# Optimization experiments

Hardware: AMD Instinct MI355X
Metric: run time of the kernel (lower is better)

Reference implementation:

```python
import jax, jax.numpy as jnp
import numpy as np

B, P, R, H, M, A = 2048, 2048, 4096, 6, 256, 256
TAU, BETA = 0.1, 5.0


def setup_inputs() -> dict:
    key = jax.random.key(0)
    ks = jax.random.split(key, 12)
    M_minus = jax.random.uniform(ks[0], (B, M), dtype=jnp.float32)
    # rank-0 actions as sparse binary mask over predicates
    action_mask = (jax.random.uniform(ks[1], (B, P)) < 0.01).astype(jnp.float32)
    # temporal gate per (microstep, rule): 0/1
    gate = (jax.random.uniform(ks[2], (B, R)) < 0.7).astype(jnp.float32)
    body_idx = jax.random.randint(ks[3], (R, H), 0, P, dtype=jnp.int32)
    body_mask = (jax.random.uniform(ks[4], (R, H)) < 0.6).astype(jnp.float32)
    body_mask = body_mask.at[:, 0].set(1.0)  # every rule has >=1 body atom
    head_idx = jax.random.randint(ks[5], (R,), 0, P, dtype=jnp.int32)
    mental_pos = jnp.arange(M, dtype=jnp.int32)  # mental predicates occupy first M slots
    rtype = jax.random.randint(ks[6], (R,), 0, 3)
    is_toM = (rtype <= 1).astype(jnp.float32)   # A->M or M->M rules
    is_toA = (rtype == 2).astype(jnp.float32)   # M->A rules
    Gamma_AtoM = 0.1 * jax.random.normal(ks[7], (R, M), dtype=jnp.float32)
    Gamma_MtoA = 0.1 * jax.random.normal(ks[8], (R, A), dtype=jnp.float32)
    b = -2.0 * jnp.ones((A,), dtype=jnp.float32)
    w = 0.2 * jax.random.normal(ks[9], (A, M), dtype=jnp.float32)
    return {"M_minus": M_minus, "action_mask": action_mask, "gate": gate,
            "body_mask": body_mask, "is_toM": is_toM, "is_toA": is_toA,
            "Gamma_AtoM": Gamma_AtoM, "Gamma_MtoA": Gamma_MtoA, "b": b, "w": w,
            "body_idx": body_idx, "head_idx": head_idx, "mental_pos": mental_pos}


def reference(M_minus, action_mask, gate, body_mask, is_toM, is_toA,
              Gamma_AtoM, Gamma_MtoA, b, w, body_idx, head_idx, mental_pos):
    Mclip = jnp.clip(M_minus, 0.0, 1.0)                       # [B,M]
    # build_val_for_microstep: scatter mental vals, set rank-0 actions to 1
    val = jnp.zeros((B, P), dtype=M_minus.dtype).at[:, mental_pos].set(Mclip)
    val = jnp.maximum(val, action_mask)                        # [B,P]

    # eval_clause_exact: soft-AND (soft-min, temperature tau) over body atoms
    body_vals = val[:, body_idx]                               # [B,R,H] gather
    v = jnp.where(body_mask > 0, body_vals, 1e4)               # padded slots never min
    g_body = -TAU * jax.nn.logsumexp(-v / TAU, axis=-1)        # [B,R]
    g = g_body * gate                                          # temporal gate

    # per-head clause aggregation: g_head = (1/beta) logsumexp_{r:head(r)=p} beta*g_r
    def seg_lse(gb):  # gb: [R]
        mx = jax.ops.segment_max(BETA * gb, head_idx, num_segments=P)
        mx_safe = jnp.where(mx > -1e30, mx, 0.0)
        s = jax.ops.segment_sum(jnp.exp(BETA * gb - mx_safe[head_idx]),
                                head_idx, num_segments=P)
        lse = (mx_safe + jnp.log(jnp.maximum(s, 1e-30))) / BETA
        return jnp.where(s > 0, lse, -1e9)
    g_head = jax.vmap(seg_lse)(g)                              # [B,P]

    mental_mask = jnp.zeros((P,), dtype=val.dtype).at[mental_pos].set(1.0)
    val_new = jnp.where(mental_mask > 0, jnp.maximum(val, g_head), val)

    # S_j(t) = relu(sum over A->M/M->M rules gamma_AtoM[r] * g_r)
    S = jax.nn.relu(jnp.einsum('br,rm->bm', g * is_toM, Gamma_AtoM))  # [B,M]
    # lambda_k(t) = softplus(b + w@M) + relu(sum over M->A rules gamma_MtoA[r]*g_r)
    lam_ment = jax.nn.softplus(b + Mclip @ w.T)                # [B,A]
    lam_logic = jax.nn.relu(jnp.einsum('br,ra->ba', g * is_toA, Gamma_MtoA))
    lam = lam_ment + lam_logic
    return jnp.concatenate([val_new, S, lam], axis=-1)         # [B, P+M+A]
```

## Files before the change

### kernel.cpp

```cpp
#include <hip/hip_runtime.h>

typedef __attribute__((ext_vector_type(8))) short short8;
typedef __attribute__((ext_vector_type(4))) float f32x4;

#define B_DIM 2048
#define P_DIM 2048
#define R_DIM 4096
#define H_DIM 6
#define M_DIM 256
#define A_DIM 256
#define OUT_STRIDE 2560
#define NB 2

#define C1 14.426950408889634f
#define K2 0.06931471805599453f
#define C2 7.213475204444817f
#define K3 0.13862943611198906f

static __device__ __forceinline__ float fexp2(float x) { return __builtin_amdgcn_exp2f(x); }
static __device__ __forceinline__ float flog2(float x) { return __builtin_amdgcn_logf(x); }

static __device__ __forceinline__ unsigned short f2bf(float f) {
    unsigned u = __builtin_bit_cast(unsigned, f);
    u += 0x7fffu + ((u >> 16) & 1u);
    return (unsigned short)(u >> 16);
}

__global__ __launch_bounds__(64) void prep_meta(
    const int* __restrict__ bidx, const float* __restrict__ bmask,
    const int* __restrict__ hidx, uint4* __restrict__ meta)
{
    const int r = blockIdx.x * 64 + threadIdx.x;
    const int* bi = bidx + r * H_DIM;
    const float* bm = bmask + r * H_DIM;
    unsigned s[H_DIM];
    #pragma unroll
    for (int h = 0; h < H_DIM; h++)
        s[h] = (bm[h] > 0.0f) ? (unsigned)bi[h] : 2048u;
    const int hh = hidx[r];
    unsigned sh = (hh < M_DIM) ? (unsigned)hh : 0xFFFFu;
    uint4 m;
    m.x = s[0] | (s[1] << 16);
    m.y = s[2] | (s[3] << 16);
    m.z = s[4] | (s[5] << 16);
    m.w = sh;
    meta[r] = m;
}

__global__ __launch_bounds__(1024, 8) void main_fused(
    const float* __restrict__ M_minus, const float* __restrict__ amask,
    const float* __restrict__ gate,    const uint4* __restrict__ meta,
    const float* __restrict__ GA, const float* __restrict__ GB,
    const float* __restrict__ isM, const float* __restrict__ isA,
    const float* __restrict__ w,
    unsigned short* __restrict__ GAT, unsigned short* __restrict__ GBT,
    unsigned short* __restrict__ wb,
    unsigned short* __restrict__ g_bf, unsigned short* __restrict__ mclip_bf,
    float* __restrict__ outp)
{
    __shared__ __align__(16) union SM {
        struct {
            float2 vrow2[2052];
            float shead[NB][M_DIM];
        } mf;
        float prep[4][32][33];
    } sm;
    const int bid = blockIdx.x;
    const int tid = threadIdx.x;
    const int b0 = bid * NB;

    if (bid < 576) {
        const int s = tid >> 8, lt = tid & 255;
        const int u = bid * 4 + s;
        if (u < 2048) {
            const int which = u >> 10;
            const int rem = u & 1023;
            const float* src = which ? GB : GA;
            const float* scv = which ? isA : isM;
            const int r0 = (rem >> 3) * 32;
            const int n0 = (rem & 7) * 32;
            const int tx = lt & 31, ty = lt >> 5;
            #pragma unroll
            for (int q = 0; q < 4; q++) {
                int rr = ty + q * 8;
                sm.prep[s][rr][tx] = scv[r0 + rr] * src[(size_t)(r0 + rr) * 256 + n0 + tx];
            }
        } else {
            const int i = (u - 2048) * 256 + lt;
            wb[i] = f2bf(w[i]);
        }
        __syncthreads();
        if (u < 2048) {
            const int which = u >> 10;
            const int rem = u & 1023;
            unsigned short* dst = which ? GBT : GAT;
            const int r0 = (rem >> 3) * 32;
            const int n0 = (rem & 7) * 32;
            const int tx = lt & 31, ty = lt >> 5;
            #pragma unroll
            for (int q = 0; q < 4; q++) {
                int nn = ty + q * 8;
                dst[(size_t)(n0 + nn) * R_DIM + r0 + tx] = f2bf(sm.prep[s][tx][nn]);
            }
        }
        __syncthreads();
    }

    if (tid < NB * M_DIM) sm.mf.shead[tid >> 8][tid & 255] = 0.0f;
    if (tid == 0) sm.mf.vrow2[2048] = make_float2(-1.0e9f, -1.0e9f);

    {
        const int p0 = tid * 2;
        float2 a0 = *(const float2*)(amask + (size_t)b0 * P_DIM + p0);
        float2 a1 = *(const float2*)(amask + (size_t)(b0 + 1) * P_DIM + p0);
        if (tid < M_DIM / 2) {
            float2 m0 = *(const float2*)(M_minus + (size_t)b0 * M_DIM + p0);
            float2 m1 = *(const float2*)(M_minus + (size_t)(b0 + 1) * M_DIM + p0);
            float mc00 = fminf(fmaxf(m0.x, 0.0f), 1.0f);
            float mc01 = fminf(fmaxf(m0.y, 0.0f), 1.0f);
            float mc10 = fminf(fmaxf(m1.x, 0.0f), 1.0f);
            float mc11 = fminf(fmaxf(m1.y, 0.0f), 1.0f);
            ushort2 w0; w0.x = f2bf(mc00); w0.y = f2bf(mc01);
            ushort2 w1; w1.x = f2bf(mc10); w1.y = f2bf(mc11);
            *(ushort2*)(mclip_bf + (size_t)b0 * M_DIM + p0) = w0;
            *(ushort2*)(mclip_bf + (size_t)(b0 + 1) * M_DIM + p0) = w1;
            a0.x = fmaxf(mc00, a0.x); a0.y = fmaxf(mc01, a0.y);
            a1.x = fmaxf(mc10, a1.x); a1.y = fmaxf(mc11, a1.y);
        }
        float4 yq;
        yq.x = -C1 * a0.x; yq.y = -C1 * a1.x;
        yq.z = -C1 * a0.y; yq.w = -C1 * a1.y;
        *(float4*)&sm.mf.vrow2[p0] = yq;
    }
    __syncthreads();

    const float* g0p = gate + (size_t)b0 * R_DIM;
    const float* g1p = gate + (size_t)(b0 + 1) * R_DIM;
    unsigned short* o0p = g_bf + (size_t)b0 * R_DIM;
    unsigned short* o1p = g_bf + (size_t)(b0 + 1) * R_DIM;

    uint4 mc = meta[tid];
    float ga = g0p[tid], gb = g1p[tid];
    #pragma unroll
    for (int it = 0; it < R_DIM / 1024; it++) {
        const int rr = tid + it * 1024;
        uint4 mn = mc; float gan = ga, gbn = gb;
        if (it < R_DIM / 1024 - 1) {
            mn  = meta[rr + 1024];
            gan = g0p[rr + 1024];
            gbn = g1p[rr + 1024];
        }
        const int i0 = mc.x & 0xFFFF, i1 = mc.x >> 16;
        const int i2 = mc.y & 0xFFFF, i3 = mc.y >> 16;
        const int i4 = mc.z & 0xFFFF, i5 = mc.z >> 16;
        const int hh = mc.w & 0xFFFF;
        float2 v0 = sm.mf.vrow2[i0], v1 = sm.mf.vrow2[i1], v2 = sm.mf.vrow2[i2];
        float2 v3 = sm.mf.vrow2[i3], v4 = sm.mf.vrow2[i4], v5 = sm.mf.vrow2[i5];

        float ym0 = fmaxf(fmaxf(fmaxf(v0.x, v1.x), fmaxf(v2.x, v3.x)), fmaxf(v4.x, v5.x));
        float ym1 = fmaxf(fmaxf(fmaxf(v0.y, v1.y), fmaxf(v2.y, v3.y)), fmaxf(v4.y, v5.y));
        float s0 = fexp2(v0.x - ym0) + fexp2(v1.x - ym0) + fexp2(v2.x - ym0)
                 + fexp2(v3.x - ym0) + fexp2(v4.x - ym0) + fexp2(v5.x - ym0);
        float s1 = fexp2(v0.y - ym1) + fexp2(v1.y - ym1) + fexp2(v2.y - ym1)
                 + fexp2(v3.y - ym1) + fexp2(v4.y - ym1) + fexp2(v5.y - ym1);
        float gg0 = (ym0 + flog2(s0)) * (-K2 * ga);
        float gg1 = (ym1 + flog2(s1)) * (-K2 * gb);
        o0p[rr] = f2bf(gg0);
        o1p[rr] = f2bf(gg1);
        if (hh < M_DIM) {
            atomicAdd(&sm.mf.shead[0][hh], fexp2(gg0 * C2));
            atomicAdd(&sm.mf.shead[1][hh], fexp2(gg1 * C2));
        }
        mc = mn; ga = gan; gb = gbn;
    }
    __syncthreads();

    {
        const int p0 = tid * 2;
        float4 yq = *(const float4*)&sm.mf.vrow2[p0];
        float v00 = -K2 * yq.x, v10 = -K2 * yq.y;
        float v01 = -K2 * yq.z, v11 = -K2 * yq.w;
        if (tid < M_DIM / 2) {
            float s00 = sm.mf.shead[0][p0], s01 = sm.mf.shead[0][p0 + 1];
            float s10 = sm.mf.shead[1][p0], s11 = sm.mf.shead[1][p0 + 1];
            if (s00 > 0.0f) v00 = fmaxf(v00, K3 * flog2(s00));
            if (s01 > 0.0f) v01 = fmaxf(v01, K3 * flog2(s01));
            if (s10 > 0.0f) v10 = fmaxf(v10, K3 * flog2(s10));
            if (s11 > 0.0f) v11 = fmaxf(v11, K3 * flog2(s11));
        }
        *(float2*)(outp + (size_t)b0 * OUT_STRIDE + p0)       = make_float2(v00, v01);
        *(float2*)(outp + (size_t)(b0 + 1) * OUT_STRIDE + p0) = make_float2(v10, v11);
    }
}

__device__ __forceinline__ void stage16(unsigned short* lds,
                                        const unsigned short* gsrc,
                                        int K, int c)
{
    const int row = c >> 4, slot = c & 15;
    const int k8 = slot ^ (row & 15);
    __builtin_amdgcn_global_load_lds(
        (const __attribute__((address_space(1))) void*)(gsrc + (size_t)row * K + k8 * 8),
        (__attribute__((address_space(3))) void*)(lds + c * 8), 16, 0, 0);
}

__global__ __launch_bounds__(256) void gemm_all(
    const unsigned short* __restrict__ g_bf,
    const unsigned short* __restrict__ GAT,
    const unsigned short* __restrict__ mclip,
    const unsigned short* __restrict__ w_bf,
    float* __restrict__ mainp, float* __restrict__ lamp)
{
    __shared__ __align__(16) unsigned short Alds[128 * 128];
    __shared__ __align__(16) unsigned short Blds[64 * 128];
    const int bid = blockIdx.x;
    const int tid = threadIdx.x;
    const int lane = tid & 63, wid = tid >> 6;
    const int wr = wid >> 1, wc = wid & 1;

    if (bid < 512) {
        const int m0 = (bid & 15) * 128;
        const int n0 = ((bid >> 4) & 7) * 64;
        const int z  = bid >> 7;
        const int K = R_DIM, Kc = R_DIM / 4, k0 = z * Kc, NS = 512;
        float* part = mainp + (size_t)z * B_DIM * NS;
        f32x4 acc[4][2] = {};

        for (int kt = 0; kt < Kc; kt += 128) {
            const unsigned short* Ab = g_bf + (size_t)m0 * K + k0 + kt;
            const unsigned short* Bb = GAT  + (size_t)n0 * K + k0 + kt;
            #pragma unroll
            for (int q = 0; q < 8; q++) stage16(Alds, Ab, K, tid + q * 256);
            #pragma unroll
            for (int q = 0; q < 4; q++) stage16(Blds, Bb, K, tid + q * 256);
            __syncthreads();
            #pragma unroll
            for (int ks = 0; ks < 4; ks++) {
                const int k8 = ks * 4 + (lane >> 4);
                const int ra = wr * 64 + (lane & 15);
                const int rb = wc * 32 + (lane & 15);
                const int sa = (k8 ^ (ra & 15)) << 3;
                const int sb = (k8 ^ (rb & 15)) << 3;
                short8 a0 = *(const short8*)&Alds[(ra)      * 128 + sa];
                short8 a1 = *(const short8*)&Alds[(ra + 16) * 128 + sa];
                short8 a2 = *(const short8*)&Alds[(ra + 32) * 128 + sa];
                short8 a3 = *(const short8*)&Alds[(ra + 48) * 128 + sa];
                short8 b0 = *(const short8*)&Blds[(rb)      * 128 + sb];
                short8 b1 = *(const short8*)&Blds[(rb + 16) * 128 + sb];
                acc[0][0] = __builtin_amdgcn_mfma_f32_16x16x32_bf16(a0, b0, acc[0][0], 0, 0, 0);
                acc[0][1] = __builtin_amdgcn_mfma_f32_16x16x32_bf16(a0, b1, acc[0][1], 0, 0, 0);
                acc[1][0] = __builtin_amdgcn_mfma_f32_16x16x32_bf16(a1, b0, acc[1][0], 0, 0, 0);
                acc[1][1] = __builtin_amdgcn_mfma_f32_16x16x32_bf16(a1, b1, acc[1][1], 0, 0, 0);
                acc[2][0] = __builtin_amdgcn_mfma_f32_16x16x32_bf16(a2, b0, acc[2][0], 0, 0, 0);
                acc[2][1] = __builtin_amdgcn_mfma_f32_16x16x32_bf16(a2, b1, acc[2][1], 0, 0, 0);
                acc[3][0] = __builtin_amdgcn_mfma_f32_16x16x32_bf16(a3, b0, acc[3][0], 0, 0, 0);
                acc[3][1] = __builtin_amdgcn_mfma_f32_16x16x32_bf16(a3, b1, acc[3][1], 0, 0, 0);
            }
            __syncthreads();
        }
        const int rbase = (lane >> 4) * 4;
        const int cbase = lane & 15;
        #pragma unroll
        for (int i = 0; i < 4; i++) {
            #pragma unroll
            for (int j = 0; j < 2; j++) {
                const int gn = n0 + wc * 32 + j * 16 + cbase;
                #pragma unroll
                for (int q = 0; q < 4; q++) {
                    const int gm = m0 + wr * 64 + i * 16 + rbase + q;
                    part[(size_t)gm * NS + gn] = acc[i][j][q];
                }
            }
        }
    } else {
        const int l = bid - 512;
        const int m0 = (l & 31) * 64;
        const int n0 = ((l >> 5) & 3) * 64;
        const int z  = l >> 7;
        const int K = M_DIM, Kc = M_DIM / 2, k0 = z * Kc, NS = A_DIM;
        float* part = lamp + (size_t)z * B_DIM * NS;
        f32x4 acc[2][2] = {};

        const unsigned short* Ab = mclip + (size_t)m0 * K + k0;
        const unsigned short* Bb = w_bf  + (size_t)n0 * K + k0;
        #pragma unroll
        for (int q = 0; q < 4; q++) {
            stage16(Alds, Ab, K, tid + q * 256);
            stage16(Blds, Bb, K, tid + q * 256);
        }
        __syncthreads();
        #pragma unroll
        for (int ks = 0; ks < 4; ks++) {
            const int k8 = ks * 4 + (lane >> 4);
            const int r0a = wr * 32 + (lane & 15);
            const int r0b = wc * 32 + (lane & 15);
            const int sa = (k8 ^ (r0a & 15)) << 3;
            const int sb = (k8 ^ (r0b & 15)) << 3;
            short8 a0 = *(const short8*)&Alds[(r0a)      * 128 + sa];
            short8 a1 = *(const short8*)&Alds[(r0a + 16) * 128 + sa];
            short8 b0 = *(const short8*)&Blds[(r0b)      * 128 + sb];
            short8 b1 = *(const short8*)&Blds[(r0b + 16) * 128 + sb];
            acc[0][0] = __builtin_amdgcn_mfma_f32_16x16x32_bf16(a0, b0, acc[0][0], 0, 0, 0);
            acc[0][1] = __builtin_amdgcn_mfma_f32_16x16x32_bf16(a0, b1, acc[0][1], 0, 0, 0);
            acc[1][0] = __builtin_amdgcn_mfma_f32_16x16x32_bf16(a1, b0, acc[1][0], 0, 0, 0);
            acc[1][1] = __builtin_amdgcn_mfma_f32_16x16x32_bf16(a1, b1, acc[1][1], 0, 0, 0);
        }
        const int rbase = (lane >> 4) * 4;
        const int cbase = lane & 15;
        #pragma unroll
        for (int i = 0; i < 2; i++) {
            #pragma unroll
            for (int j = 0; j < 2; j++) {
                const int gn = n0 + wc * 32 + j * 16 + cbase;
                #pragma unroll
                for (int q = 0; q < 4; q++) {
                    const int gm = m0 + wr * 32 + i * 16 + rbase + q;
                    part[(size_t)gm * NS + gn] = acc[i][j][q];
                }
            }
        }
    }
}

__global__ __launch_bounds__(256) void epilogue(
    const float* __restrict__ mainpart, const float* __restrict__ lampart,
    const float* __restrict__ bvec, float* __restrict__ outp)
{
    const int idx = blockIdx.x * 256 + threadIdx.x;
    const int m = idx >> 7, n4 = idx & 127;
    const size_t mb = (size_t)m * 128 + n4;
    const size_t zs = (size_t)B_DIM * 128;
    float4 s = ((const float4*)mainpart)[mb];
    #pragma unroll
    for (int z = 1; z < 4; z++) {
        float4 t = ((const float4*)mainpart)[mb + z * zs];
        s.x += t.x; s.y += t.y; s.z += t.z; s.w += t.w;
    }
    s.x = fmaxf(s.x, 0.0f); s.y = fmaxf(s.y, 0.0f);
    s.z = fmaxf(s.z, 0.0f); s.w = fmaxf(s.w, 0.0f);
    if (n4 >= 64) {
        const int na = n4 - 64;
        const size_t lb = (size_t)m * 64 + na;
        float4 l0 = ((const float4*)lampart)[lb];
        float4 l1 = ((const float4*)lampart)[lb + (size_t)B_DIM * 64];
        float4 bb = ((const float4*)bvec)[na];
        float x0 = bb.x + l0.x + l1.x, x1 = bb.y + l0.y + l1.y;
        float x2 = bb.z + l0.z + l1.z, x3 = bb.w + l0.w + l1.w;
        s.x += (x0 > 20.0f) ? x0 : log1pf(__expf(x0));
        s.y += (x1 > 20.0f) ? x1 : log1pf(__expf(x1));
        s.z += (x2 > 20.0f) ? x2 : log1pf(__expf(x2));
        s.w += (x3 > 20.0f) ? x3 : log1pf(__expf(x3));
    }
    ((float4*)(outp + (size_t)m * OUT_STRIDE + 2048))[n4] = s;
}

extern "C" void kernel_launch(void* const* d_in, const int* in_sizes, int n_in,
                              void* d_out, int out_size, void* d_ws, size_t ws_size,
                              hipStream_t stream)
{
    const float* M_minus = (const float*)d_in[0];
    const float* amask   = (const float*)d_in[1];
    const float* gate    = (const float*)d_in[2];
    const float* bmask   = (const float*)d_in[3];
    const float* isM     = (const float*)d_in[4];
    const float* isA     = (const float*)d_in[5];
    const float* GA      = (const float*)d_in[6];
    const float* GB      = (const float*)d_in[7];
    const float* bvec    = (const float*)d_in[8];
    const float* w       = (const float*)d_in[9];
    const int*   bidx    = (const int*)d_in[10];
    const int*   hidx    = (const int*)d_in[11];
    float* outp = (float*)d_out;

    char* ws = (char*)d_ws;
    unsigned short* g_bf   = (unsigned short*)(ws + 0);
    unsigned short* GAT    = (unsigned short*)(ws + (16u<<20));
    unsigned short* GBT    = (unsigned short*)(ws + (18u<<20));
    unsigned short* w_bf   = (unsigned short*)(ws + (20u<<20));
    uint4*          meta   = (uint4*)(ws + (20u<<20) + (256u<<10));
    unsigned short* mclip  = (unsigned short*)(ws + (21u<<20));
    float*          mainp  = (float*)(ws + (22u<<20));
    float*          lamp   = (float*)(ws + (38u<<20));

    prep_meta<<<dim3(R_DIM / 64), dim3(64), 0, stream>>>(bidx, bmask, hidx, meta);
    main_fused<<<dim3(B_DIM / NB), dim3(1024), 0, stream>>>(
        M_minus, amask, gate, meta, GA, GB, isM, isA, w,
        GAT, GBT, w_bf, g_bf, mclip, outp);
    gemm_all<<<dim3(768), dim3(256), 0, stream>>>(
        g_bf, GAT, mclip, w_bf, mainp, lamp);
    epilogue<<<dim3((B_DIM * 128) / 256), dim3(256), 0, stream>>>(
        mainp, lamp, bvec, outp);
}
```

Measured before the change: 50.74 us.

## Store split-K partials in fp16, drop softmin max-shift, and swizzle GEMM block order

The GEMM's split-K partial sums are now written to the workspace as fp16 instead of fp32, and the epilogue reads them back as fp16. This halves the intermediate write and read traffic. The soft-min logsumexp no longer subtracts the running max before exponentiating, which saves the max reductions and subtractions but risks overflow or underflow depending on the value range. The main GEMM block index is also permuted so neighbouring blocks take different K-slices and tiles, with the aim of changing cache locality. The fp16 partials lose precision and could overflow for large accumulations.

```diff
diff --git a/kernel.cpp b/kernel.cpp
--- a/kernel.cpp
+++ b/kernel.cpp
@@ -24,6 +24,12 @@
     unsigned u = __builtin_bit_cast(unsigned, f);
     u += 0x7fffu + ((u >> 16) & 1u);
     return (unsigned short)(u >> 16);
+}
+static __device__ __forceinline__ unsigned short f2h(float f) {
+    return __builtin_bit_cast(unsigned short, (_Float16)f);
+}
+static __device__ __forceinline__ float h2f(unsigned short u) {
+    return (float)__builtin_bit_cast(_Float16, u);
 }
 
 __global__ __launch_bounds__(64) void prep_meta(
@@ -157,14 +163,12 @@
         float2 v0 = sm.mf.vrow2[i0], v1 = sm.mf.vrow2[i1], v2 = sm.mf.vrow2[i2];
         float2 v3 = sm.mf.vrow2[i3], v4 = sm.mf.vrow2[i4], v5 = sm.mf.vrow2[i5];
 
-        float ym0 = fmaxf(fmaxf(fmaxf(v0.x, v1.x), fmaxf(v2.x, v3.x)), fmaxf(v4.x, v5.x));
-        float ym1 = fmaxf(fmaxf(fmaxf(v0.y, v1.y), fmaxf(v2.y, v3.y)), fmaxf(v4.y, v5.y));
-        float s0 = fexp2(v0.x - ym0) + fexp2(v1.x - ym0) + fexp2(v2.x - ym0)
-                 + fexp2(v3.x - ym0) + fexp2(v4.x - ym0) + fexp2(v5.x - ym0);
-        float s1 = fexp2(v0.y - ym1) + fexp2(v1.y - ym1) + fexp2(v2.y - ym1)
-                 + fexp2(v3.y - ym1) + fexp2(v4.y - ym1) + fexp2(v5.y - ym1);
-        float gg0 = (ym0 + flog2(s0)) * (-K2 * ga);
-        float gg1 = (ym1 + flog2(s1)) * (-K2 * gb);
+        float s0 = fexp2(v0.x) + fexp2(v1.x) + fexp2(v2.x)
+                 + fexp2(v3.x) + fexp2(v4.x) + fexp2(v5.x);
+        float s1 = fexp2(v0.y) + fexp2(v1.y) + fexp2(v2.y)
+                 + fexp2(v3.y) + fexp2(v4.y) + fexp2(v5.y);
+        float gg0 = flog2(s0) * (-K2 * ga);
+        float gg1 = flog2(s1) * (-K2 * gb);
         o0p[rr] = f2bf(gg0);
         o1p[rr] = f2bf(gg1);
         if (hh < M_DIM) {
@@ -209,7 +213,7 @@
     const unsigned short* __restrict__ GAT,
     const unsigned short* __restrict__ mclip,
     const unsigned short* __restrict__ w_bf,
-    float* __restrict__ mainp, float* __restrict__ lamp)
+    unsigned short* __restrict__ mainp, unsigned short* __restrict__ lamp)
 {
     __shared__ __align__(16) unsigned short Alds[128 * 128];
     __shared__ __align__(16) unsigned short Blds[64 * 128];
@@ -219,11 +223,12 @@
     const int wr = wid >> 1, wc = wid & 1;
 
     if (bid < 512) {
-        const int m0 = (bid & 15) * 128;
-        const int n0 = ((bid >> 4) & 7) * 64;
-        const int z  = bid >> 7;
+        const int l = (bid & 7) * 64 + (bid >> 3);
+        const int m0 = (l & 15) * 128;
+        const int n0 = ((l >> 4) & 7) * 64;
+        const int z  = l >> 7;
         const int K = R_DIM, Kc = R_DIM / 4, k0 = z * Kc, NS = 512;
-        float* part = mainp + (size_t)z * B_DIM * NS;
+        unsigned short* part = mainp + (size_t)z * B_DIM * NS;
         f32x4 acc[4][2] = {};
 
         for (int kt = 0; kt < Kc; kt += 128) {
@@ -268,7 +273,7 @@
                 #pragma unroll
                 for (int q = 0; q < 4; q++) {
                     const int gm = m0 + wr * 64 + i * 16 + rbase + q;
-                    part[(size_t)gm * NS + gn] = acc[i][j][q];
+                    part[(size_t)gm * NS + gn] = f2h(acc[i][j][q]);
                 }
             }
         }
@@ -278,7 +283,7 @@
         const int n0 = ((l >> 5) & 3) * 64;
         const int z  = l >> 7;
         const int K = M_DIM, Kc = M_DIM / 2, k0 = z * Kc, NS = A_DIM;
-        float* part = lamp + (size_t)z * B_DIM * NS;
+        unsigned short* part = lamp + (size_t)z * B_DIM * NS;
         f32x4 acc[2][2] = {};
 
         const unsigned short* Ab = mclip + (size_t)m0 * K + k0;
@@ -315,7 +320,7 @@
                 #pragma unroll
                 for (int q = 0; q < 4; q++) {
                     const int gm = m0 + wr * 32 + i * 16 + rbase + q;
-                    part[(size_t)gm * NS + gn] = acc[i][j][q];
+                    part[(size_t)gm * NS + gn] = f2h(acc[i][j][q]);
                 }
             }
         }
@@ -323,34 +328,39 @@
 }
 
 __global__ __launch_bounds__(256) void epilogue(
-    const float* __restrict__ mainpart, const float* __restrict__ lampart,
+    const unsigned short* __restrict__ mainpart,
+    const unsigned short* __restrict__ lampart,
     const float* __restrict__ bvec, float* __restrict__ outp)
 {
     const int idx = blockIdx.x * 256 + threadIdx.x;
     const int m = idx >> 7, n4 = idx & 127;
     const size_t mb = (size_t)m * 128 + n4;
     const size_t zs = (size_t)B_DIM * 128;
-    float4 s = ((const float4*)mainpart)[mb];
+    float sx = 0.0f, sy = 0.0f, sz = 0.0f, sw = 0.0f;
     #pragma unroll
-    for (int z = 1; z < 4; z++) {
-        float4 t = ((const float4*)mainpart)[mb + z * zs];
-        s.x += t.x; s.y += t.y; s.z += t.z; s.w += t.w;
-    }
-    s.x = fmaxf(s.x, 0.0f); s.y = fmaxf(s.y, 0.0f);
-    s.z = fmaxf(s.z, 0.0f); s.w = fmaxf(s.w, 0.0f);
+    for (int z = 0; z < 4; z++) {
+        ushort4 t = ((const ushort4*)mainpart)[mb + z * zs];
+        sx += h2f(t.x); sy += h2f(t.y); sz += h2f(t.z); sw += h2f(t.w);
+    }
+    sx = fmaxf(sx, 0.0f); sy = fmaxf(sy, 0.0f);
+    sz = fmaxf(sz, 0.0f); sw = fmaxf(sw, 0.0f);
     if (n4 >= 64) {
         const int na = n4 - 64;
         const size_t lb = (size_t)m * 64 + na;
-        float4 l0 = ((const float4*)lampart)[lb];
-        float4 l1 = ((const float4*)lampart)[lb + (size_t)B_DIM * 64];
+        const size_t ls = (size_t)B_DIM * 64;
+        ushort4 u0 = ((const ushort4*)lampart)[lb];
+        ushort4 u1 = ((const ushort4*)lampart)[lb + ls];
         float4 bb = ((const float4*)bvec)[na];
-        float x0 = bb.x + l0.x + l1.x, x1 = bb.y + l0.y + l1.y;
-        float x2 = bb.z + l0.z + l1.z, x3 = bb.w + l0.w + l1.w;
-        s.x += (x0 > 20.0f) ? x0 : log1pf(__expf(x0));
-        s.y += (x1 > 20.0f) ? x1 : log1pf(__expf(x1));
-        s.z += (x2 > 20.0f) ? x2 : log1pf(__expf(x2));
-        s.w += (x3 > 20.0f) ? x3 : log1pf(__expf(x3));
-    }
+        float x0 = bb.x + h2f(u0.x) + h2f(u1.x);
+        float x1 = bb.y + h2f(u0.y) + h2f(u1.y);
+        float x2 = bb.z + h2f(u0.z) + h2f(u1.z);
+        float x3 = bb.w + h2f(u0.w) + h2f(u1.w);
+        sx += (x0 > 20.0f) ? x0 : log1pf(__expf(x0));
+        sy += (x1 > 20.0f) ? x1 : log1pf(__expf(x1));
+        sz += (x2 > 20.0f) ? x2 : log1pf(__expf(x2));
+        sw += (x3 > 20.0f) ? x3 : log1pf(__expf(x3));
+    }
+    float4 s; s.x = sx; s.y = sy; s.z = sz; s.w = sw;
     ((float4*)(outp + (size_t)m * OUT_STRIDE + 2048))[n4] = s;
 }
 
@@ -379,8 +389,8 @@
     unsigned short* w_bf   = (unsigned short*)(ws + (20u<<20));
     uint4*          meta   = (uint4*)(ws + (20u<<20) + (256u<<10));
     unsigned short* mclip  = (unsigned short*)(ws + (21u<<20));
-    float*          mainp  = (float*)(ws + (22u<<20));
-    float*          lamp   = (float*)(ws + (38u<<20));
+    unsigned short* mainp  = (unsigned short*)(ws + (22u<<20));
+    unsigned short* lamp   = (unsigned short*)(ws + (38u<<20));
 
     prep_meta<<<dim3(R_DIM / 64), dim3(64), 0, stream>>>(bidx, bmask, hidx, meta);
     main_fused<<<dim3(B_DIM / NB), dim3(1024), 0, stream>>>(
```

New measurement: 49.34 us. 2.8% less time.
